# Kernel tuning notes

Hardware: AMD Instinct MI355X
Metric: run time of the kernel (lower is better)

## Reference

```python
import jax, jax.numpy as jnp
import numpy as np

N = 100_000      # nodes
F_IN = 256       # input features
HID = 256        # hidden dim
C = 40           # classes
E = 1_600_000    # edges
BN_EPS = 1e-5


def setup_inputs() -> dict:
    key = jax.random.key(0)
    ks = jax.random.split(key, 8)
    x = jax.random.normal(ks[0], (N, F_IN), dtype=jnp.float32)
    edge_index = jax.random.randint(ks[1], (2, E), 0, N)
    W1 = jax.random.normal(ks[2], (F_IN, HID), dtype=jnp.float32) / np.sqrt(F_IN)
    b1 = jnp.zeros((HID,), jnp.float32)
    gamma = jnp.ones((HID,), jnp.float32)
    beta = jnp.zeros((HID,), jnp.float32)
    W2 = jax.random.normal(ks[3], (HID, C), dtype=jnp.float32) / np.sqrt(HID)
    b2 = jnp.zeros((C,), jnp.float32)
    return {"x": x, "edge_index": edge_index, "W1": W1, "b1": b1,
            "gamma": gamma, "beta": beta, "W2": W2, "b2": b2}


def _gcn_propagate(h, src, dst, norm):
    # out[dst] += norm * h[src]   (symmetric-normalized aggregation, self-loops included)
    msg = norm[:, None] * h[src]                       # [E+N, D]
    return jax.ops.segment_sum(msg, dst, num_segments=N)


def reference(x, edge_index, W1, b1, gamma, beta, W2, b2):
    loops = jnp.arange(N, dtype=edge_index.dtype)
    src = jnp.concatenate([edge_index[0], loops])      # add self-loops (PyG GCNConv)
    dst = jnp.concatenate([edge_index[1], loops])
    deg = jax.ops.segment_sum(jnp.ones_like(dst, jnp.float32), dst, num_segments=N)
    dinv = jnp.where(deg > 0, jax.lax.rsqrt(deg), 0.0)
    norm = dinv[src] * dinv[dst]

    # Layer 1: GCNConv (linear without bias -> propagate -> + bias)
    h = _gcn_propagate(x @ W1, src, dst, norm) + b1    # [N, HID]
    # BatchNorm1d over nodes (training-style batch statistics, biased variance)
    mu = h.mean(axis=0)
    var = h.var(axis=0)
    h = (h - mu) * jax.lax.rsqrt(var + BN_EPS) * gamma + beta
    h = jax.nn.relu(h)                                 # dropout is identity in eval

    # Layer 2: GCNConv -> log_softmax
    out = _gcn_propagate(h @ W2, src, dst, norm) + b2  # [N, C]
    return jax.nn.log_softmax(out, axis=1)
```

## Files before the change

kernel.cpp:

```cpp
#include <hip/hip_runtime.h>
#include <math.h>

#define N_NODES 100000
#define F_IN    256
#define HID     256
#define C_OUT   40
#define N_EDGES 1600000
#define BN_EPS  1e-5f

#define SCAN_CHUNK  1024
#define SCAN_BLOCKS ((N_NODES + SCAN_CHUNK - 1) / SCAN_CHUNK)
#define CNT_BLOCKS  ((N_EDGES + 255) / 256)
#define NPASS 8
#define DRANGE (N_NODES / NPASS)

typedef __attribute__((ext_vector_type(8))) short short8;
typedef __attribute__((ext_vector_type(8))) unsigned short ushort8v;
typedef __attribute__((ext_vector_type(4))) float f32x4;

static __device__ __forceinline__ unsigned short f2bf(float f) {
    unsigned int u = __float_as_uint(f);
    unsigned int r = u + 0x7FFFu + ((u >> 16) & 1u);
    return (unsigned short)(r >> 16);
}
static __device__ __forceinline__ float bf2f(unsigned short b) {
    return __uint_as_float(((unsigned int)b) << 16);
}

__global__ void count_dst_castw(const int* __restrict__ dst, int* cnt,
                                const float* __restrict__ W1, const float* __restrict__ W2,
                                unsigned short* __restrict__ w1t, unsigned short* __restrict__ w2t) {
    int b = blockIdx.x, t = threadIdx.x;
    if (b < CNT_BLOCKS) {
        int i = b * 256 + t;
        if (i < N_EDGES) atomicAdd(&cnt[dst[i]], 1);
    } else if (b < CNT_BLOCKS + 256) {
        int n = b - CNT_BLOCKS;
        w1t[(size_t)n * 256 + t] = f2bf(W1[(size_t)t * 256 + n]);
    } else {
        int n = b - CNT_BLOCKS - 256;
        w2t[(size_t)n * 256 + t] = (n < C_OUT) ? f2bf(W2[(size_t)t * C_OUT + n]) : (unsigned short)0;
    }
}

__global__ __launch_bounds__(256) void scan_partial(const int* __restrict__ cnt,
                                                    int* blocksum) {
    __shared__ int red[256];
    int t = threadIdx.x;
    int base = blockIdx.x * SCAN_CHUNK + t * 4;
    int s = 0;
    if (base + 3 < N_NODES) {
        int4 c = *(const int4*)(cnt + base);
        s = c.x + c.y + c.z + c.w + 4;
    } else {
        for (int q = 0; q < 4; q++) if (base + q < N_NODES) s += cnt[base + q] + 1;
    }
    red[t] = s;
    __syncthreads();
    for (int off = 128; off > 0; off >>= 1) {
        if (t < off) red[t] += red[t + off];
        __syncthreads();
    }
    if (t == 0) blocksum[blockIdx.x] = red[0];
}

__global__ __launch_bounds__(128) void scan_blocksums(const int* __restrict__ blocksum,
                                                      int* blockoff, int* rowoff) {
    __shared__ int sm[128];
    int t = threadIdx.x;
    int v = (t < SCAN_BLOCKS) ? blocksum[t] : 0;
    sm[t] = v;
    __syncthreads();
    for (int off = 1; off < 128; off <<= 1) {
        int u = (t >= off) ? sm[t - off] : 0;
        __syncthreads();
        sm[t] += u;
        __syncthreads();
    }
    if (t < SCAN_BLOCKS) blockoff[t] = sm[t] - v;
    if (t == 0) rowoff[N_NODES] = N_EDGES + N_NODES;
}

__global__ __launch_bounds__(256) void scan_write_init(const int* __restrict__ cnt,
                                                       const int* __restrict__ blockoff,
                                                       int* rowoff, float* dinv,
                                                       int* cursor, int* csr) {
    __shared__ int red[256];
    int t = threadIdx.x;
    int base = blockIdx.x * SCAN_CHUNK + t * 4;
    int c[4] = {0, 0, 0, 0};
    if (base + 3 < N_NODES) {
        int4 cc = *(const int4*)(cnt + base);
        c[0] = cc.x + 1; c[1] = cc.y + 1; c[2] = cc.z + 1; c[3] = cc.w + 1;
    } else {
        for (int q = 0; q < 4; q++) c[q] = (base + q < N_NODES) ? cnt[base + q] + 1 : 0;
    }
    int s = c[0] + c[1] + c[2] + c[3];
    red[t] = s;
    __syncthreads();
    for (int off = 1; off < 256; off <<= 1) {
        int u = (t >= off) ? red[t - off] : 0;
        __syncthreads();
        red[t] += u;
        __syncthreads();
    }
    int run = blockoff[blockIdx.x] + red[t] - s;
    for (int q = 0; q < 4; q++) {
        int idx = base + q;
        if (idx < N_NODES) {
            rowoff[idx] = run;
            dinv[idx] = rsqrtf((float)c[q]);
            csr[run] = idx;
            cursor[idx] = 1;
            run += c[q];
        }
    }
}

__global__ void scatter_mp(const int* __restrict__ src,
                           const int* __restrict__ dst,
                           const int* __restrict__ rowoff,
                           int* cursor, int* csr) {
    int p = blockIdx.x / CNT_BLOCKS;
    int e = (blockIdx.x - p * CNT_BLOCKS) * 256 + threadIdx.x;
    if (e < N_EDGES) {
        int d = dst[e];
        if (d / DRANGE == p) {
            int pos = rowoff[d] + atomicAdd(&cursor[d], 1);
            csr[pos] = src[e];
        }
    }
}

#define LDK 56
__global__ __launch_bounds__(256) void gemm1_mfma(const float* __restrict__ x,
                                                  const unsigned short* __restrict__ w1t,
                                                  const float* __restrict__ dinv,
                                                  unsigned short* __restrict__ hs, int M) {
    __shared__ unsigned short As[64][LDK];
    __shared__ unsigned short Bs[256][LDK];
    int tid = threadIdx.x;
    int wave = tid >> 6, lane = tid & 63;
    int m0 = blockIdx.x * 64;
    f32x4 acc[4][4] = {};

    int ar = tid >> 2, ac = (tid & 3) * 8;
    int brow = tid;
    int gr = m0 + ar;
    bool rowok = gr < M;
    const float* xrow = x + (size_t)gr * 256 + ac;
    const unsigned short* wrow = w1t + (size_t)brow * 256;

    float4 pa = make_float4(0.f,0.f,0.f,0.f), pb = pa;
    if (rowok) { pa = *(const float4*)(xrow); pb = *(const float4*)(xrow + 4); }
    ushort8v rb0 = *(const ushort8v*)(wrow);
    ushort8v rb1 = *(const ushort8v*)(wrow + 8);
    ushort8v rb2 = *(const ushort8v*)(wrow + 16);
    ushort8v rb3 = *(const ushort8v*)(wrow + 24);

    for (int k0 = 0; k0 < 256; k0 += 32) {
        {
            ushort8v u;
            u[0] = f2bf(pa.x); u[1] = f2bf(pa.y); u[2] = f2bf(pa.z); u[3] = f2bf(pa.w);
            u[4] = f2bf(pb.x); u[5] = f2bf(pb.y); u[6] = f2bf(pb.z); u[7] = f2bf(pb.w);
            if (!rowok) {
#pragma unroll
                for (int q = 0; q < 8; q++) u[q] = 0;
            }
            *(ushort8v*)&As[ar][ac] = u;
        }
        *(ushort8v*)&Bs[brow][0]  = rb0;
        *(ushort8v*)&Bs[brow][8]  = rb1;
        *(ushort8v*)&Bs[brow][16] = rb2;
        *(ushort8v*)&Bs[brow][24] = rb3;
        __syncthreads();
        if (k0 + 32 < 256) {
            if (rowok) {
                pa = *(const float4*)(xrow + k0 + 32);
                pb = *(const float4*)(xrow + k0 + 36);
            }
            const unsigned short* p = wrow + k0 + 32;
            rb0 = *(const ushort8v*)(p);
            rb1 = *(const ushort8v*)(p + 8);
            rb2 = *(const ushort8v*)(p + 16);
            rb3 = *(const ushort8v*)(p + 24);
        }
        int fr = lane & 15, fk = (lane >> 4) * 8;
        short8 a[4], b[4];
#pragma unroll
        for (int mt = 0; mt < 4; mt++) a[mt] = *(short8*)&As[mt * 16 + fr][fk];
#pragma unroll
        for (int nt = 0; nt < 4; nt++) b[nt] = *(short8*)&Bs[wave * 64 + nt * 16 + fr][fk];
#pragma unroll
        for (int mt = 0; mt < 4; mt++)
#pragma unroll
            for (int nt = 0; nt < 4; nt++)
                acc[mt][nt] = __builtin_amdgcn_mfma_f32_16x16x32_bf16(a[mt], b[nt], acc[mt][nt], 0, 0, 0);
        __syncthreads();
    }
    int fr = lane & 15, fg = lane >> 4;
#pragma unroll
    for (int mt = 0; mt < 4; mt++) {
#pragma unroll
        for (int r = 0; r < 4; r++) {
            int row = m0 + mt * 16 + fg * 4 + r;
            if (row < M) {
                float dv = dinv[row];
#pragma unroll
                for (int nt = 0; nt < 4; nt++) {
                    int col = wave * 64 + nt * 16 + fr;
                    hs[(size_t)row * 256 + col] = f2bf(acc[mt][nt][r] * dv);
                }
            }
        }
    }
}

__global__ __launch_bounds__(256) void agg256(const int* __restrict__ rowoff,
                                              const int* __restrict__ csr,
                                              const unsigned short* __restrict__ hs,
                                              const float* __restrict__ dinv,
                                              unsigned short* __restrict__ hagg) {
    int g = blockIdx.x * blockDim.x + threadIdx.x;
    int wid = g >> 6, lane = g & 63;
    if (wid >= N_NODES) return;
    int half = lane >> 5;
    int c8 = (lane & 31) * 8;
    int beg = rowoff[wid], end = rowoff[wid + 1];
    float acc[8] = {0.f, 0.f, 0.f, 0.f, 0.f, 0.f, 0.f, 0.f};
    int j = beg;
    if (j + 7 < end) {
        int sxA[4];
        ushort8v uA[4];
#pragma unroll
        for (int q = 0; q < 4; q++) sxA[q] = csr[j + 2 * q + half];
#pragma unroll
        for (int q = 0; q < 4; q++) uA[q] = *(const ushort8v*)(hs + (size_t)sxA[q] * 256 + c8);
        j += 8;
        while (j + 7 < end) {
            int sxB[4];
            ushort8v uB[4];
#pragma unroll
            for (int q = 0; q < 4; q++) sxB[q] = csr[j + 2 * q + half];
#pragma unroll
            for (int q = 0; q < 4; q++) uB[q] = *(const ushort8v*)(hs + (size_t)sxB[q] * 256 + c8);
#pragma unroll
            for (int q = 0; q < 4; q++)
#pragma unroll
                for (int e = 0; e < 8; e++) acc[e] += bf2f(uA[q][e]);
#pragma unroll
            for (int q = 0; q < 4; q++) uA[q] = uB[q];
            j += 8;
        }
#pragma unroll
        for (int q = 0; q < 4; q++)
#pragma unroll
            for (int e = 0; e < 8; e++) acc[e] += bf2f(uA[q][e]);
    }
    if (j + 3 < end) {
        int s0 = csr[j + half];
        int s1 = csr[j + 2 + half];
        ushort8v u0 = *(const ushort8v*)(hs + (size_t)s0 * 256 + c8);
        ushort8v u1 = *(const ushort8v*)(hs + (size_t)s1 * 256 + c8);
#pragma unroll
        for (int e = 0; e < 8; e++) acc[e] += bf2f(u0[e]) + bf2f(u1[e]);
        j += 4;
    }
    if (j + 1 < end) {
        int s = csr[j + half];
        ushort8v u = *(const ushort8v*)(hs + (size_t)s * 256 + c8);
#pragma unroll
        for (int e = 0; e < 8; e++) acc[e] += bf2f(u[e]);
        j += 2;
    }
    if (j < end && half == 0) {
        int s = csr[j];
        ushort8v u = *(const ushort8v*)(hs + (size_t)s * 256 + c8);
#pragma unroll
        for (int e = 0; e < 8; e++) acc[e] += bf2f(u[e]);
    }
#pragma unroll
    for (int e = 0; e < 8; e++) acc[e] += __shfl_xor(acc[e], 32);
    float dv = dinv[wid];
    if (half == 0) {
        ushort8v o;
#pragma unroll
        for (int e = 0; e < 8; e++) o[e] = f2bf(acc[e] * dv);
        *(ushort8v*)(hagg + (size_t)wid * 256 + c8) = o;
    }
}

#define BNS_BLOCKS 1024
__global__ __launch_bounds__(256) void bn_stats_v(const unsigned short* __restrict__ h,
                                                  float* musum, float* sqsum) {
    int tid = threadIdx.x;
    int wave = tid >> 6, lane = tid & 63;
    int half = lane >> 5;
    int c8 = (lane & 31) * 8;
    int gw = blockIdx.x * 4 + wave;
    float s[8] = {0.f,0.f,0.f,0.f,0.f,0.f,0.f,0.f};
    float q2[8] = {0.f,0.f,0.f,0.f,0.f,0.f,0.f,0.f};
    for (int r = gw * 2 + half; r < N_NODES; r += BNS_BLOCKS * 4 * 2) {
        ushort8v u = *(const ushort8v*)(h + (size_t)r * 256 + c8);
#pragma unroll
        for (int e = 0; e < 8; e++) {
            float v = bf2f(u[e]);
            s[e] += v; q2[e] += v * v;
        }
    }
#pragma unroll
    for (int e = 0; e < 8; e++) {
        s[e]  += __shfl_xor(s[e], 32);
        q2[e] += __shfl_xor(q2[e], 32);
    }
    __shared__ float sS[4][256];
    __shared__ float sQ[4][256];
    if (half == 0) {
#pragma unroll
        for (int e = 0; e < 8; e++) { sS[wave][c8 + e] = s[e]; sQ[wave][c8 + e] = q2[e]; }
    }
    __syncthreads();
    float a = sS[0][tid] + sS[1][tid] + sS[2][tid] + sS[3][tid];
    float b = sQ[0][tid] + sQ[1][tid] + sQ[2][tid] + sQ[3][tid];
    atomicAdd(&musum[tid], a);
    atomicAdd(&sqsum[tid], b);
}

#define LDB2 264
__global__ __launch_bounds__(256) void gemm2_mfma(const unsigned short* __restrict__ hagg,
                                                  const unsigned short* __restrict__ w2t,
                                                  const float* __restrict__ musum,
                                                  const float* __restrict__ sqsum,
                                                  const float* __restrict__ gamma,
                                                  const float* __restrict__ beta,
                                                  const float* __restrict__ dinv,
                                                  unsigned short* __restrict__ g2b, int M) {
    __shared__ unsigned short w2s[48][LDB2];
    __shared__ unsigned short As[64][40];
    __shared__ float ss[256], sh[256];
    int tid = threadIdx.x;
    int wave = tid >> 6, lane = tid & 63;
    int m0 = blockIdx.x * 64;

    for (int i = tid; i < 48 * 32; i += 256) {
        int rrow = i >> 5, c8 = (i & 31) * 8;
        *(ushort8v*)&w2s[rrow][c8] = *(const ushort8v*)(w2t + (size_t)rrow * 256 + c8);
    }
    {
        const float invN = 1.0f / N_NODES;
        float m = musum[tid] * invN;
        float var = sqsum[tid] * invN - m * m;
        float s = gamma[tid] * rsqrtf(var + BN_EPS);
        ss[tid] = s;
        sh[tid] = beta[tid] - m * s;
    }

    f32x4 acc[3] = {};
    int arow = tid >> 2, ac0 = (tid & 3) * 8;
    int fr = lane & 15, fk = (lane >> 4) * 8;

    for (int k0 = 0; k0 < 256; k0 += 32) {
        __syncthreads();
        {
            int gr = m0 + arow;
            ushort8v u;
            if (gr < M) {
                u = *(const ushort8v*)(hagg + (size_t)gr * 256 + k0 + ac0);
#pragma unroll
                for (int q = 0; q < 8; q++) {
                    int col = k0 + ac0 + q;
                    float v = bf2f(u[q]);
                    v = fmaxf(v * ss[col] + sh[col], 0.0f);
                    u[q] = f2bf(v);
                }
            } else {
#pragma unroll
                for (int q = 0; q < 8; q++) u[q] = 0;
            }
            *(ushort8v*)&As[arow][ac0] = u;
        }
        __syncthreads();
        short8 a = *(short8*)&As[wave * 16 + fr][fk];
#pragma unroll
        for (int nt = 0; nt < 3; nt++) {
            short8 b = *(short8*)&w2s[nt * 16 + fr][k0 + fk];
            acc[nt] = __builtin_amdgcn_mfma_f32_16x16x32_bf16(a, b, acc[nt], 0, 0, 0);
        }
    }
    int fg = lane >> 4;
#pragma unroll
    for (int nt = 0; nt < 3; nt++) {
        int col = nt * 16 + fr;
        if (col < C_OUT) {
#pragma unroll
            for (int r = 0; r < 4; r++) {
                int row = m0 + wave * 16 + fg * 4 + r;
                if (row < M) g2b[(size_t)row * C_OUT + col] = f2bf(acc[nt][r] * dinv[row]);
            }
        }
    }
}

__global__ __launch_bounds__(256) void agg40_logsm(const int* __restrict__ rowoff,
                                                   const int* __restrict__ csr,
                                                   const unsigned short* __restrict__ g2b,
                                                   const float* __restrict__ dinv,
                                                   const float* __restrict__ b2,
                                                   float* __restrict__ out) {
    int gi = blockIdx.x * blockDim.x + threadIdx.x;
    int wid = gi >> 6, lane = gi & 63;
    if (wid >= N_NODES) return;
    int g = lane / 10;
    int k4 = lane - g * 10;
    bool gact = lane < 60;
    int beg = rowoff[wid], end = rowoff[wid + 1];
    int jlim = end - 1;
    float a4[4] = {0.f, 0.f, 0.f, 0.f};
    int j = beg;
    int s0 = csr[min(j + g, jlim)];
    ushort4 u0 = *(const ushort4*)(g2b + (size_t)s0 * C_OUT + k4 * 4);
    while (1) {
        int jn = j + 6;
        bool more = jn < end;
        int s1 = 0; ushort4 u1;
        if (more) {
            s1 = csr[min(jn + g, jlim)];
            u1 = *(const ushort4*)(g2b + (size_t)s1 * C_OUT + k4 * 4);
        }
        if (gact && j + g < end) {
            a4[0] += bf2f(u0.x); a4[1] += bf2f(u0.y);
            a4[2] += bf2f(u0.z); a4[3] += bf2f(u0.w);
        }
        if (!more) break;
        u0 = u1; j = jn;
    }
#pragma unroll
    for (int e = 0; e < 4; e++) {
        float t0 = __shfl(a4[e], lane + 30);
        a4[e] += t0;
    }
#pragma unroll
    for (int e = 0; e < 4; e++) {
        float t1 = __shfl(a4[e], lane + 10);
        float t2 = __shfl(a4[e], lane + 20);
        a4[e] += t1 + t2;
    }
    bool act = lane < 10;
    float dvd = dinv[wid];
    float v[4];
    float mloc = -INFINITY;
#pragma unroll
    for (int e = 0; e < 4; e++) {
        v[e] = act ? a4[e] * dvd + b2[k4 * 4 + e] : -INFINITY;
        mloc = fmaxf(mloc, v[e]);
    }
#pragma unroll
    for (int o = 32; o > 0; o >>= 1) mloc = fmaxf(mloc, __shfl_xor(mloc, o));
    float sloc = 0.f;
    if (act) {
#pragma unroll
        for (int e = 0; e < 4; e++) sloc += __expf(v[e] - mloc);
    }
#pragma unroll
    for (int o = 32; o > 0; o >>= 1) sloc += __shfl_xor(sloc, o);
    float ls = __logf(sloc);
    if (act) {
        float4 o4 = make_float4(v[0] - mloc - ls, v[1] - mloc - ls,
                                v[2] - mloc - ls, v[3] - mloc - ls);
        *(float4*)(out + (size_t)wid * C_OUT + k4 * 4) = o4;
    }
}

extern "C" void kernel_launch(void* const* d_in, const int* in_sizes, int n_in,
                              void* d_out, int out_size, void* d_ws, size_t ws_size,
                              hipStream_t stream) {
    const float* x     = (const float*)d_in[0];
    const int*   ei    = (const int*)  d_in[1];
    const float* W1    = (const float*)d_in[2];
    const float* gamma = (const float*)d_in[4];
    const float* beta  = (const float*)d_in[5];
    const float* W2    = (const float*)d_in[6];
    const float* b2    = (const float*)d_in[7];
    float* out = (float*)d_out;

    const int* src = ei;
    const int* dst = ei + N_EDGES;

    unsigned short* hs    = (unsigned short*)d_ws;
    unsigned short* hagg  = hs + (size_t)N_NODES * 256;
    unsigned short* g2b   = hagg + (size_t)N_NODES * 256;
    float*          dinv  = (float*)(g2b + (size_t)N_NODES * C_OUT);
    int*            cnt   = (int*)(dinv + N_NODES);
    int*            rowoff= cnt + N_NODES;
    int*            cursor= rowoff + N_NODES + 1;
    int*            csr   = cursor + N_NODES;
    unsigned short* w1t   = (unsigned short*)(csr + N_EDGES + N_NODES);
    unsigned short* w2t   = w1t + 65536;
    float*          musum = (float*)(w2t + 48 * 256);
    float*          sqsum = musum + 256;
    int*            blocksum = (int*)(sqsum + 256);
    int*            blockoff = blocksum + 128;

    hipMemsetAsync(cnt, 0, N_NODES * sizeof(int), stream);
    hipMemsetAsync(musum, 0, 512 * sizeof(float), stream);

    count_dst_castw<<<CNT_BLOCKS + 256 + 48, 256, 0, stream>>>(dst, cnt, W1, W2, w1t, w2t);
    scan_partial<<<SCAN_BLOCKS, 256, 0, stream>>>(cnt, blocksum);
    scan_blocksums<<<1, 128, 0, stream>>>(blocksum, blockoff, rowoff);
    scan_write_init<<<SCAN_BLOCKS, 256, 0, stream>>>(cnt, blockoff, rowoff, dinv, cursor, csr);
    scatter_mp<<<NPASS * CNT_BLOCKS, 256, 0, stream>>>(src, dst, rowoff, cursor, csr);

    gemm1_mfma<<<(N_NODES + 63) / 64, 256, 0, stream>>>(x, w1t, dinv, hs, N_NODES);

    int aggblk = (int)(((size_t)N_NODES * 64 + 255) / 256);
    agg256<<<aggblk, 256, 0, stream>>>(rowoff, csr, hs, dinv, hagg);

    bn_stats_v<<<BNS_BLOCKS, 256, 0, stream>>>(hagg, musum, sqsum);

    gemm2_mfma<<<(N_NODES + 63) / 64, 256, 0, stream>>>(hagg, w2t, musum, sqsum, gamma, beta, dinv, g2b, N_NODES);

    agg40_logsm<<<aggblk, 256, 0, stream>>>(rowoff, csr, g2b, dinv, b2, out);
}
```

Baseline: 465.8 us.

## Record per-edge rank during degree count to scatter CSR without atomics

```diff
diff --git a/kernel.cpp b/kernel.cpp
--- a/kernel.cpp
+++ b/kernel.cpp
@@ -11,8 +11,6 @@
 #define SCAN_CHUNK  1024
 #define SCAN_BLOCKS ((N_NODES + SCAN_CHUNK - 1) / SCAN_CHUNK)
 #define CNT_BLOCKS  ((N_EDGES + 255) / 256)
-#define NPASS 8
-#define DRANGE (N_NODES / NPASS)
 
 typedef __attribute__((ext_vector_type(8))) short short8;
 typedef __attribute__((ext_vector_type(8))) unsigned short ushort8v;
@@ -28,12 +26,13 @@
 }
 
 __global__ void count_dst_castw(const int* __restrict__ dst, int* cnt,
+                                int* __restrict__ rank,
                                 const float* __restrict__ W1, const float* __restrict__ W2,
                                 unsigned short* __restrict__ w1t, unsigned short* __restrict__ w2t) {
     int b = blockIdx.x, t = threadIdx.x;
     if (b < CNT_BLOCKS) {
         int i = b * 256 + t;
-        if (i < N_EDGES) atomicAdd(&cnt[dst[i]], 1);
+        if (i < N_EDGES) rank[i] = atomicAdd(&cnt[dst[i]], 1);
     } else if (b < CNT_BLOCKS + 256) {
         int n = b - CNT_BLOCKS;
         w1t[(size_t)n * 256 + t] = f2bf(W1[(size_t)t * 256 + n]);
@@ -84,7 +83,7 @@
 __global__ __launch_bounds__(256) void scan_write_init(const int* __restrict__ cnt,
                                                        const int* __restrict__ blockoff,
                                                        int* rowoff, float* dinv,
-                                                       int* cursor, int* csr) {
+                                                       int* csr) {
     __shared__ int red[256];
     int t = threadIdx.x;
     int base = blockIdx.x * SCAN_CHUNK + t * 4;
@@ -111,24 +110,20 @@
             rowoff[idx] = run;
             dinv[idx] = rsqrtf((float)c[q]);
             csr[run] = idx;
-            cursor[idx] = 1;
             run += c[q];
         }
     }
 }
 
-__global__ void scatter_mp(const int* __restrict__ src,
-                           const int* __restrict__ dst,
-                           const int* __restrict__ rowoff,
-                           int* cursor, int* csr) {
-    int p = blockIdx.x / CNT_BLOCKS;
-    int e = (blockIdx.x - p * CNT_BLOCKS) * 256 + threadIdx.x;
+__global__ __launch_bounds__(256) void scatter_rank(const int* __restrict__ src,
+                                                    const int* __restrict__ dst,
+                                                    const int* __restrict__ rank,
+                                                    const int* __restrict__ rowoff,
+                                                    int* __restrict__ csr) {
+    int e = blockIdx.x * 256 + threadIdx.x;
     if (e < N_EDGES) {
         int d = dst[e];
-        if (d / DRANGE == p) {
-            int pos = rowoff[d] + atomicAdd(&cursor[d], 1);
-            csr[pos] = src[e];
-        }
+        csr[rowoff[d] + 1 + rank[e]] = src[e];
     }
 }
 
@@ -492,23 +487,23 @@
     float*          dinv  = (float*)(g2b + (size_t)N_NODES * C_OUT);
     int*            cnt   = (int*)(dinv + N_NODES);
     int*            rowoff= cnt + N_NODES;
-    int*            cursor= rowoff + N_NODES + 1;
-    int*            csr   = cursor + N_NODES;
+    int*            csr   = rowoff + N_NODES + 1;
     unsigned short* w1t   = (unsigned short*)(csr + N_EDGES + N_NODES);
     unsigned short* w2t   = w1t + 65536;
     float*          musum = (float*)(w2t + 48 * 256);
     float*          sqsum = musum + 256;
     int*            blocksum = (int*)(sqsum + 256);
     int*            blockoff = blocksum + 128;
+    int*            rank  = (int*)hagg;
 
     hipMemsetAsync(cnt, 0, N_NODES * sizeof(int), stream);
     hipMemsetAsync(musum, 0, 512 * sizeof(float), stream);
 
-    count_dst_castw<<<CNT_BLOCKS + 256 + 48, 256, 0, stream>>>(dst, cnt, W1, W2, w1t, w2t);
+    count_dst_castw<<<CNT_BLOCKS + 256 + 48, 256, 0, stream>>>(dst, cnt, rank, W1, W2, w1t, w2t);
     scan_partial<<<SCAN_BLOCKS, 256, 0, stream>>>(cnt, blocksum);
     scan_blocksums<<<1, 128, 0, stream>>>(blocksum, blockoff, rowoff);
-    scan_write_init<<<SCAN_BLOCKS, 256, 0, stream>>>(cnt, blockoff, rowoff, dinv, cursor, csr);
-    scatter_mp<<<NPASS * CNT_BLOCKS, 256, 0, stream>>>(src, dst, rowoff, cursor, csr);
+    scan_write_init<<<SCAN_BLOCKS, 256, 0, stream>>>(cnt, blockoff, rowoff, dinv, csr);
+    scatter_rank<<<CNT_BLOCKS, 256, 0, stream>>>(src, dst, rank, rowoff, csr);
 
     gemm1_mfma<<<(N_NODES + 63) / 64, 256, 0, stream>>>(x, w1t, dinv, hs, N_NODES);
 
```

Result: faster. 416.6 us (-10.6%).
